# Performance work log

Measured on AMD Instinct MI355X. Metric: run time of the kernel, lower is better.

Reference implementation:

```python
import jax, jax.numpy as jnp
import numpy as np

N_NODES = 100000
N_EDGES = 400000
D = 128
BN_EPS = 1e-5


def setup_inputs() -> dict:
    key = jax.random.key(0)
    ks = jax.random.split(key, 8)
    lim = 1.0 / np.sqrt(D)  # torch Linear default init range
    feature = jax.random.normal(ks[0], (N_NODES, D), dtype=jnp.float32)
    edge_index = jax.random.randint(ks[1], (2, N_EDGES), 0, N_NODES, dtype=jnp.int64)
    w1 = jax.random.uniform(ks[2], (D, D), jnp.float32, -lim, lim)
    b1 = jax.random.uniform(ks[3], (D,), jnp.float32, -lim, lim)
    w2 = jax.random.uniform(ks[4], (D, D), jnp.float32, -lim, lim)
    b2 = jax.random.uniform(ks[5], (D,), jnp.float32, -lim, lim)
    gamma = jnp.ones((D,), jnp.float32)
    beta = jnp.zeros((D,), jnp.float32)
    return {"feature": feature, "edge_index": edge_index, "w1": w1, "b1": b1,
            "w2": w2, "b2": b2, "gamma": gamma, "beta": beta}


def reference(feature, edge_index, w1, b1, w2, b2, gamma, beta):
    n = feature.shape[0]
    src, dst = edge_index[0], edge_index[1]
    # GIN aggregation (eps=0): h_i = x_i + sum_{j: (j->i)} x_j
    agg = jax.ops.segment_sum(feature[src], dst, num_segments=n)
    h = feature + agg
    # 2-layer MLP: Linear -> ReLU -> Linear (torch Linear: x @ W.T + b)
    h = jnp.maximum(h @ w1.T + b1, 0.0) @ w2.T + b2
    # ReLU then BatchNorm1d (training mode: batch stats, biased variance)
    h = jnp.maximum(h, 0.0)
    mean = jnp.mean(h, axis=0)
    var = jnp.mean(jnp.square(h - mean), axis=0)
    return (h - mean) * jax.lax.rsqrt(var + BN_EPS) * gamma + beta
```

## Files before the change

kernel.cpp:

```cpp
#include <hip/hip_runtime.h>
#include <hip/hip_bf16.h>

#define DD 128
#define TM 64
#define LD 136
#define SB 128
#define GRID_MLP 1024

typedef short bf16x8 __attribute__((ext_vector_type(8)));
typedef float f32x4  __attribute__((ext_vector_type(4)));

__device__ __forceinline__ unsigned short f2bf(float f) {
  unsigned int u = __float_as_uint(f);
  u += 0x7FFFu + ((u >> 16) & 1u);
  return (unsigned short)(u >> 16);
}
__device__ __forceinline__ unsigned int pack2(float lo, float hi) {
  return (unsigned int)f2bf(lo) | ((unsigned int)f2bf(hi) << 16);
}
__device__ __forceinline__ float bf2f(unsigned short u) {
  union { unsigned int i; float f; } x; x.i = ((unsigned int)u) << 16; return x.f;
}

__global__ __launch_bounds__(256) void k_init(const float* __restrict__ w1,
                                              const float* __restrict__ w2,
                                              unsigned short* __restrict__ wbf1,
                                              unsigned short* __restrict__ wbf2,
                                              int* __restrict__ cnt, int nrows) {
  int i = blockIdx.x * 256 + threadIdx.x;
  if (i < nrows) cnt[i] = 0;
  if (i < DD * DD) { wbf1[i] = f2bf(w1[i]); wbf2[i] = f2bf(w2[i]); }
}

__global__ __launch_bounds__(256) void k_hist(const int* __restrict__ ei, int* __restrict__ cnt,
                                              int ne) {
  int e = blockIdx.x * 256 + threadIdx.x;
  if (e < ne) atomicAdd(&cnt[ei[ne + e]], 1);
}

__global__ __launch_bounds__(256) void k_scan1(const int* __restrict__ cnt,
                                               int* __restrict__ bsum, int n) {
  __shared__ int red[256];
  int b = blockIdx.x, t = threadIdx.x;
  int chunk = (n + SB - 1) / SB;
  int lo = b * chunk, hi = min(n, lo + chunk);
  int s = 0;
  for (int i = lo + t; i < hi; i += 256) s += cnt[i];
  red[t] = s;
  __syncthreads();
  for (int off = 128; off; off >>= 1) {
    if (t < off) red[t] += red[t + off];
    __syncthreads();
  }
  if (t == 0) bsum[b] = red[0];
}

__global__ __launch_bounds__(256) void k_scan3(const int* __restrict__ cnt,
                                               const int* __restrict__ bsum,
                                               int* __restrict__ ofs, int* __restrict__ cur,
                                               int n) {
  __shared__ int red[256];
  __shared__ int sbs[SB];
  int b = blockIdx.x, t = threadIdx.x;

  int ov = (t < SB) ? bsum[t] : 0;
  if (t < SB) sbs[t] = ov;
  __syncthreads();
  for (int off = 1; off < SB; off <<= 1) {
    int v = (t < SB && t >= off) ? sbs[t - off] : 0;
    __syncthreads();
    if (t < SB) sbs[t] += v;
    __syncthreads();
  }
  if (t < SB) sbs[t] -= ov;
  __syncthreads();
  int base = sbs[b];
  if (b == SB - 1 && t == SB - 1) ofs[n] = sbs[t] + ov;

  int chunk  = (n + SB - 1) / SB;
  int tchunk = (chunk + 255) / 256;
  int blo = b * chunk, bhi = min(n, blo + chunk);
  int lo = blo + t * tchunk, hi = min(bhi, lo + tchunk);
  int s = 0;
  for (int i = lo; i < hi; ++i) s += cnt[i];
  int mine = s;
  red[t] = s;
  __syncthreads();
  for (int off = 1; off < 256; off <<= 1) {
    int v = (t >= off) ? red[t - off] : 0;
    __syncthreads();
    red[t] += v;
    __syncthreads();
  }
  int run = base + red[t] - mine;
  for (int i = lo; i < hi; ++i) {
    int c = cnt[i];
    ofs[i] = run; cur[i] = run;
    run += c;
  }
}

__global__ __launch_bounds__(256) void k_fill(const int* __restrict__ ei, int* __restrict__ cur,
                                              int* __restrict__ csr, int ne) {
  int e = blockIdx.x * 256 + threadIdx.x;
  if (e >= ne) return;
  int pos = atomicAdd(&cur[ei[ne + e]], 1);
  csr[pos] = ei[e];
}

__global__ __launch_bounds__(256) void k_agg(
    const float* __restrict__ feat, const int* __restrict__ ofs, const int* __restrict__ csr,
    unsigned short* __restrict__ agg, int nrows)
{
  int t = blockIdx.x * 256 + threadIdx.x;
  int row = t >> 4;
  if (row >= nrows) return;
  int c = (t & 15) * 8;
  const float* fr = feat + (long long)row * DD + c;
  float4 a0 = *reinterpret_cast<const float4*>(fr);
  float4 b0 = *reinterpret_cast<const float4*>(fr + 4);
  float4 a1 = make_float4(0.f, 0.f, 0.f, 0.f);
  float4 b1 = make_float4(0.f, 0.f, 0.f, 0.f);
  int o0 = ofs[row], o1 = ofs[row + 1];
  int j = o0;
  for (; j + 2 <= o1; j += 2) {
    const float* f0 = feat + (long long)csr[j]     * DD + c;
    const float* f1 = feat + (long long)csr[j + 1] * DD + c;
    float4 x0 = *reinterpret_cast<const float4*>(f0);
    float4 y0 = *reinterpret_cast<const float4*>(f0 + 4);
    float4 x1 = *reinterpret_cast<const float4*>(f1);
    float4 y1 = *reinterpret_cast<const float4*>(f1 + 4);
    a0.x += x0.x; a0.y += x0.y; a0.z += x0.z; a0.w += x0.w;
    b0.x += y0.x; b0.y += y0.y; b0.z += y0.z; b0.w += y0.w;
    a1.x += x1.x; a1.y += x1.y; a1.z += x1.z; a1.w += x1.w;
    b1.x += y1.x; b1.y += y1.y; b1.z += y1.z; b1.w += y1.w;
  }
  if (j < o1) {
    const float* f0 = feat + (long long)csr[j] * DD + c;
    float4 x0 = *reinterpret_cast<const float4*>(f0);
    float4 y0 = *reinterpret_cast<const float4*>(f0 + 4);
    a0.x += x0.x; a0.y += x0.y; a0.z += x0.z; a0.w += x0.w;
    b0.x += y0.x; b0.y += y0.y; b0.z += y0.z; b0.w += y0.w;
  }
  a0.x += a1.x; a0.y += a1.y; a0.z += a1.z; a0.w += a1.w;
  b0.x += b1.x; b0.y += b1.y; b0.z += b1.z; b0.w += b1.w;
  uint4 u;
  u.x = pack2(a0.x, a0.y); u.y = pack2(a0.z, a0.w);
  u.z = pack2(b0.x, b0.y); u.w = pack2(b0.z, b0.w);
  *reinterpret_cast<uint4*>(agg + (long long)row * DD + c) = u;
}

__global__ __launch_bounds__(256) void k_mlp(
    unsigned short* hb,
    const unsigned short* __restrict__ wbf1, const float* __restrict__ b1,
    const unsigned short* __restrict__ wbf2, const float* __restrict__ b2,
    float* __restrict__ partial, int nrows, int ntiles)
{
  __shared__ unsigned short ldsH[TM * LD];
  __shared__ unsigned short ldsH2[TM * LD];
  const int tid  = threadIdx.x;
  const int wave = tid >> 6, lane = tid & 63;
  const int q = lane >> 4, l16 = lane & 15;
  const int col0 = wave * 32;

  bf16x8 bw1[2][4], bw2[2][4];
  float bias1[2], bias2[2];
  for (int n = 0; n < 2; ++n) {
    int jc = col0 + n * 16 + l16;
    bias1[n] = b1[jc];
    bias2[n] = b2[jc];
    for (int kk = 0; kk < 4; ++kk) {
      bw1[n][kk] = *reinterpret_cast<const bf16x8*>(wbf1 + jc * DD + kk * 32 + q * 8);
      bw2[n][kk] = *reinterpret_cast<const bf16x8*>(wbf2 + jc * DD + kk * 32 + q * 8);
    }
  }

  float fs[2] = {0.f, 0.f}, fs2[2] = {0.f, 0.f};

  for (int tile = blockIdx.x; tile < ntiles; tile += GRID_MLP) {
    const int row0 = tile * TM;

    for (int it = 0; it < 4; ++it) {
      int idx = it * 2048 + tid * 8;
      int r = idx >> 7, c = idx & 127;
      int row = row0 + r;
      uint4 u = make_uint4(0u, 0u, 0u, 0u);
      if (row < nrows)
        u = *reinterpret_cast<const uint4*>(hb + (long long)row * DD + c);
      *reinterpret_cast<uint4*>(&ldsH[r * LD + c]) = u;
    }
    __syncthreads();

    f32x4 acc[4][2];
    const f32x4 zero = {0.f, 0.f, 0.f, 0.f};
    for (int m = 0; m < 4; ++m) for (int n = 0; n < 2; ++n) acc[m][n] = zero;

    for (int kk = 0; kk < 4; ++kk) {
      bf16x8 aF[4];
      for (int m = 0; m < 4; ++m)
        aF[m] = *reinterpret_cast<const bf16x8*>(&ldsH[(m * 16 + l16) * LD + kk * 32 + q * 8]);
      for (int m = 0; m < 4; ++m)
        for (int n = 0; n < 2; ++n)
          acc[m][n] = __builtin_amdgcn_mfma_f32_16x16x32_bf16(aF[m], bw1[n][kk], acc[m][n], 0, 0, 0);
    }

    for (int m = 0; m < 4; ++m)
      for (int n = 0; n < 2; ++n)
        for (int r = 0; r < 4; ++r) {
          float v = fmaxf(acc[m][n][r] + bias1[n], 0.f);
          ldsH2[(m * 16 + q * 4 + r) * LD + (col0 + n * 16 + l16)] = f2bf(v);
        }
    __syncthreads();

    for (int m = 0; m < 4; ++m) for (int n = 0; n < 2; ++n) acc[m][n] = zero;

    for (int kk = 0; kk < 4; ++kk) {
      bf16x8 aF[4];
      for (int m = 0; m < 4; ++m)
        aF[m] = *reinterpret_cast<const bf16x8*>(&ldsH2[(m * 16 + l16) * LD + kk * 32 + q * 8]);
      for (int m = 0; m < 4; ++m)
        for (int n = 0; n < 2; ++n)
          acc[m][n] = __builtin_amdgcn_mfma_f32_16x16x32_bf16(aF[m], bw2[n][kk], acc[m][n], 0, 0, 0);
    }

    for (int m = 0; m < 4; ++m)
      for (int n = 0; n < 2; ++n) {
        int col = col0 + n * 16 + l16;
        for (int r = 0; r < 4; ++r) {
          int rl = m * 16 + q * 4 + r;
          float v = fmaxf(acc[m][n][r] + bias2[n], 0.f);
          ldsH[rl * LD + col] = f2bf(v);
          if (row0 + rl < nrows) { fs[n] += v; fs2[n] += v * v; }
        }
      }
    __syncthreads();

    for (int it = 0; it < 4; ++it) {
      int idx = it * 2048 + tid * 8;
      int r = idx >> 7, c = idx & 127;
      int row = row0 + r;
      if (row < nrows)
        *reinterpret_cast<uint4*>(hb + (long long)row * DD + c) =
            *reinterpret_cast<const uint4*>(&ldsH[r * LD + c]);
    }
    __syncthreads();
  }

  for (int off = 16; off < 64; off <<= 1)
    for (int n = 0; n < 2; ++n) {
      fs[n]  += __shfl_xor(fs[n], off);
      fs2[n] += __shfl_xor(fs2[n], off);
    }
  if (q == 0) {
    float* pb = partial + (long long)blockIdx.x * 256;
    for (int n = 0; n < 2; ++n) {
      int col = col0 + n * 16 + l16;
      pb[col]       = fs[n];
      pb[128 + col] = fs2[n];
    }
  }
}

__global__ __launch_bounds__(256) void k_stats(const float* __restrict__ partial,
                                               const float* __restrict__ gamma,
                                               const float* __restrict__ beta,
                                               float* __restrict__ scsh, int nrows) {
  __shared__ float red[256];
  int t = threadIdx.x;
  float s = 0.f;
  for (int b = 0; b < GRID_MLP; ++b) s += partial[(long long)b * 256 + t];
  red[t] = s;
  __syncthreads();
  if (t < 128) {
    float mean = red[t] / (float)nrows;
    float var  = fmaxf(red[128 + t] / (float)nrows - mean * mean, 0.f);
    float inv  = rsqrtf(var + 1e-5f);
    float sc   = gamma[t] * inv;
    scsh[t]       = sc;
    scsh[128 + t] = beta[t] - mean * sc;
  }
}

__global__ __launch_bounds__(256) void k_bn(const unsigned short* __restrict__ hbuf,
                                            float* __restrict__ out,
                                            const float* __restrict__ scsh,
                                            long long total8) {
  long long t = (long long)blockIdx.x * 256 + threadIdx.x;
  if (t >= total8) return;
  int c0 = (int)((t * 8) & 127);
  float4 sa = *reinterpret_cast<const float4*>(scsh + c0);
  float4 sb = *reinterpret_cast<const float4*>(scsh + c0 + 4);
  float4 ha = *reinterpret_cast<const float4*>(scsh + 128 + c0);
  float4 hb = *reinterpret_cast<const float4*>(scsh + 132 + c0);
  uint4 u = *reinterpret_cast<const uint4*>(hbuf + t * 8);
  float4 a, b;
  a.x = bf2f((unsigned short)(u.x & 0xFFFF)) * sa.x + ha.x;
  a.y = bf2f((unsigned short)(u.x >> 16))    * sa.y + ha.y;
  a.z = bf2f((unsigned short)(u.y & 0xFFFF)) * sa.z + ha.z;
  a.w = bf2f((unsigned short)(u.y >> 16))    * sa.w + ha.w;
  b.x = bf2f((unsigned short)(u.z & 0xFFFF)) * sb.x + hb.x;
  b.y = bf2f((unsigned short)(u.z >> 16))    * sb.y + hb.y;
  b.z = bf2f((unsigned short)(u.w & 0xFFFF)) * sb.z + hb.z;
  b.w = bf2f((unsigned short)(u.w >> 16))    * sb.w + hb.w;
  float* of = out + t * 8;
  *reinterpret_cast<float4*>(of)     = a;
  *reinterpret_cast<float4*>(of + 4) = b;
}

extern "C" void kernel_launch(void* const* d_in, const int* in_sizes, int n_in,
                              void* d_out, int out_size, void* d_ws, size_t ws_size,
                              hipStream_t stream) {
  const float* feat  = (const float*)d_in[0];
  const int*   eidx  = (const int*)d_in[1];
  const float* w1    = (const float*)d_in[2];
  const float* b1    = (const float*)d_in[3];
  const float* w2    = (const float*)d_in[4];
  const float* b2    = (const float*)d_in[5];
  const float* gamma = (const float*)d_in[6];
  const float* beta  = (const float*)d_in[7];
  float* out = (float*)d_out;

  const int nrows  = in_sizes[0] / DD;
  const int ne     = in_sizes[1] / 2;
  const int ntiles = (nrows + TM - 1) / TM;

  int* base = (int*)d_ws;
  unsigned short* wbf1 = (unsigned short*)base;
  unsigned short* wbf2 = (unsigned short*)(base + 8192);
  float* scsh  = (float*)(base + 16384);
  int*   ofs   = base + 16384 + 256;
  int*   cur   = ofs + (nrows + 1);
  int*   csr   = cur + nrows;
  int*   bsum  = csr + ne;
  float* partial = (float*)(bsum + SB);
  int*   cnt   = (int*)(partial + (size_t)GRID_MLP * 256);
  long long w_off = (long long)(cnt + nrows - base);
  w_off = (w_off + 3) & ~3LL;
  unsigned short* hbuf = (unsigned short*)(base + w_off);

  const long long total8 = (long long)nrows * DD / 8;
  const int agg_blocks  = (nrows * 16 + 255) / 256;
  const int init_blocks = (nrows + 255) / 256;

  k_init <<<init_blocks,                  256, 0, stream>>>(w1, w2, wbf1, wbf2, cnt, nrows);
  k_hist <<<(ne + 255) / 256,             256, 0, stream>>>(eidx, cnt, ne);
  k_scan1<<<SB,                           256, 0, stream>>>(cnt, bsum, nrows);
  k_scan3<<<SB,                           256, 0, stream>>>(cnt, bsum, ofs, cur, nrows);
  k_fill <<<(ne + 255) / 256,             256, 0, stream>>>(eidx, cur, csr, ne);
  k_agg  <<<agg_blocks,                   256, 0, stream>>>(feat, ofs, csr, hbuf, nrows);
  k_mlp  <<<GRID_MLP,                     256, 0, stream>>>(hbuf, wbf1, b1, wbf2, b2,
                                                            partial, nrows, ntiles);
  k_stats<<<1,                            256, 0, stream>>>(partial, gamma, beta, scsh, nrows);
  k_bn   <<<(int)((total8 + 255) / 256),  256, 0, stream>>>(hbuf, out, scsh, total8);
}
```

Measured before the change: 246.3 us.

## Load MLP input fragments directly from global and parallelize BN stats reduction

The first MLP GEMM now reads its A fragments straight from global memory into registers instead of staging the tile through LDS. This removes one LDS round trip and one barrier per tile, and the end-of-tile sync is dropped as well. The stats kernel now launches one block per feature column with a shared-memory tree reduction, replacing a single block that looped serially over all partials. The trade-off is that direct global fragment loads are less coalesced than the previous staged copy.

```diff
diff --git a/kernel.cpp b/kernel.cpp
--- a/kernel.cpp
+++ b/kernel.cpp
@@ -156,7 +156,7 @@
     const unsigned short* __restrict__ wbf2, const float* __restrict__ b2,
     float* __restrict__ partial, int nrows, int ntiles)
 {
-  __shared__ unsigned short ldsH[TM * LD];
+  __shared__ unsigned short ldsP[TM * LD];
   __shared__ unsigned short ldsH2[TM * LD];
   const int tid  = threadIdx.x;
   const int wave = tid >> 6, lane = tid & 63;
@@ -175,31 +175,29 @@
     }
   }
 
+  const bf16x8 zf = {0, 0, 0, 0, 0, 0, 0, 0};
   float fs[2] = {0.f, 0.f}, fs2[2] = {0.f, 0.f};
 
   for (int tile = blockIdx.x; tile < ntiles; tile += GRID_MLP) {
     const int row0 = tile * TM;
-
-    for (int it = 0; it < 4; ++it) {
-      int idx = it * 2048 + tid * 8;
-      int r = idx >> 7, c = idx & 127;
-      int row = row0 + r;
-      uint4 u = make_uint4(0u, 0u, 0u, 0u);
-      if (row < nrows)
-        u = *reinterpret_cast<const uint4*>(hb + (long long)row * DD + c);
-      *reinterpret_cast<uint4*>(&ldsH[r * LD + c]) = u;
-    }
-    __syncthreads();
 
     f32x4 acc[4][2];
     const f32x4 zero = {0.f, 0.f, 0.f, 0.f};
     for (int m = 0; m < 4; ++m) for (int n = 0; n < 2; ++n) acc[m][n] = zero;
 
+    #pragma unroll
     for (int kk = 0; kk < 4; ++kk) {
       bf16x8 aF[4];
+      #pragma unroll
+      for (int m = 0; m < 4; ++m) {
+        int row = row0 + m * 16 + l16;
+        aF[m] = (row < nrows)
+            ? *reinterpret_cast<const bf16x8*>(hb + (long long)row * DD + kk * 32 + q * 8)
+            : zf;
+      }
+      #pragma unroll
       for (int m = 0; m < 4; ++m)
-        aF[m] = *reinterpret_cast<const bf16x8*>(&ldsH[(m * 16 + l16) * LD + kk * 32 + q * 8]);
-      for (int m = 0; m < 4; ++m)
+        #pragma unroll
         for (int n = 0; n < 2; ++n)
           acc[m][n] = __builtin_amdgcn_mfma_f32_16x16x32_bf16(aF[m], bw1[n][kk], acc[m][n], 0, 0, 0);
     }
@@ -214,11 +212,15 @@
 
     for (int m = 0; m < 4; ++m) for (int n = 0; n < 2; ++n) acc[m][n] = zero;
 
+    #pragma unroll
     for (int kk = 0; kk < 4; ++kk) {
       bf16x8 aF[4];
+      #pragma unroll
       for (int m = 0; m < 4; ++m)
         aF[m] = *reinterpret_cast<const bf16x8*>(&ldsH2[(m * 16 + l16) * LD + kk * 32 + q * 8]);
+      #pragma unroll
       for (int m = 0; m < 4; ++m)
+        #pragma unroll
         for (int n = 0; n < 2; ++n)
           acc[m][n] = __builtin_amdgcn_mfma_f32_16x16x32_bf16(aF[m], bw2[n][kk], acc[m][n], 0, 0, 0);
     }
@@ -229,7 +231,7 @@
         for (int r = 0; r < 4; ++r) {
           int rl = m * 16 + q * 4 + r;
           float v = fmaxf(acc[m][n][r] + bias2[n], 0.f);
-          ldsH[rl * LD + col] = f2bf(v);
+          ldsP[rl * LD + col] = f2bf(v);
           if (row0 + rl < nrows) { fs[n] += v; fs2[n] += v * v; }
         }
       }
@@ -241,9 +243,8 @@
       int row = row0 + r;
       if (row < nrows)
         *reinterpret_cast<uint4*>(hb + (long long)row * DD + c) =
-            *reinterpret_cast<const uint4*>(&ldsH[r * LD + c]);
-    }
-    __syncthreads();
+            *reinterpret_cast<const uint4*>(&ldsP[r * LD + c]);
+    }
   }
 
   for (int off = 16; off < 64; off <<= 1)
@@ -265,19 +266,27 @@
                                                const float* __restrict__ gamma,
                                                const float* __restrict__ beta,
                                                float* __restrict__ scsh, int nrows) {
-  __shared__ float red[256];
+  __shared__ float s0[256], s1[256];
+  int c = blockIdx.x;
   int t = threadIdx.x;
-  float s = 0.f;
-  for (int b = 0; b < GRID_MLP; ++b) s += partial[(long long)b * 256 + t];
-  red[t] = s;
-  __syncthreads();
-  if (t < 128) {
-    float mean = red[t] / (float)nrows;
-    float var  = fmaxf(red[128 + t] / (float)nrows - mean * mean, 0.f);
+  float a = 0.f, b = 0.f;
+  for (int r = t; r < GRID_MLP; r += 256) {
+    a += partial[(long long)r * 256 + c];
+    b += partial[(long long)r * 256 + 128 + c];
+  }
+  s0[t] = a; s1[t] = b;
+  __syncthreads();
+  for (int off = 128; off; off >>= 1) {
+    if (t < off) { s0[t] += s0[t + off]; s1[t] += s1[t + off]; }
+    __syncthreads();
+  }
+  if (t == 0) {
+    float mean = s0[0] / (float)nrows;
+    float var  = fmaxf(s1[0] / (float)nrows - mean * mean, 0.f);
     float inv  = rsqrtf(var + 1e-5f);
-    float sc   = gamma[t] * inv;
-    scsh[t]       = sc;
-    scsh[128 + t] = beta[t] - mean * sc;
+    float sc   = gamma[c] * inv;
+    scsh[c]       = sc;
+    scsh[128 + c] = beta[c] - mean * sc;
   }
 }
 
@@ -350,6 +359,6 @@
   k_agg  <<<agg_blocks,                   256, 0, stream>>>(feat, ofs, csr, hbuf, nrows);
   k_mlp  <<<GRID_MLP,                     256, 0, stream>>>(hbuf, wbf1, b1, wbf2, b2,
                                                             partial, nrows, ntiles);
-  k_stats<<<1,                            256, 0, stream>>>(partial, gamma, beta, scsh, nrows);
+  k_stats<<<128,                          256, 0, stream>>>(partial, gamma, beta, scsh, nrows);
   k_bn   <<<(int)((total8 + 255) / 256),  256, 0, stream>>>(hbuf, out, scsh, total8);
 }
```

Result: faster. 229.8 us (-6.7%).
